# Performance work log

Measured on AMD Instinct MI355X. Metric: run time of the kernel, lower is better.

The kernel has to match this reference:

```python
import jax, jax.numpy as jnp
import numpy as np


def setup_inputs() -> dict:
    key = jax.random.key(0)
    ks = jax.random.split(key, 4)
    B, T, D, H, E = 4, 2048, 1024, 4096, 8
    s = 0.02
    x = jax.random.normal(ks[0], (B, T, D), dtype=jnp.float32)
    Wr = jax.random.normal(ks[1], (D, E), dtype=jnp.float32) * s
    br = jnp.zeros((E,), dtype=jnp.float32)
    W1 = jax.random.normal(ks[2], (E, D, H), dtype=jnp.float32) * s
    b1 = jnp.zeros((E, H), dtype=jnp.float32)
    W2 = jax.random.normal(ks[3], (E, H, D), dtype=jnp.float32) * s
    b2 = jnp.zeros((E, D), dtype=jnp.float32)
    return {"x": x, "Wr": Wr, "br": br, "W1": W1, "b1": b1, "W2": W2, "b2": b2}


def reference(x, Wr, br, W1, b1, W2, b2):
    # Router: top-1 selection
    logits = jnp.einsum('btd,de->bte', x, Wr) + br            # [B,T,E]
    probs = jax.nn.softmax(logits, axis=-1)                   # [B,T,E]
    expert_idx = jnp.argmax(probs, axis=-1)                   # [B,T] int
    E = W1.shape[0]
    onehot = jax.nn.one_hot(expert_idx, E, dtype=x.dtype)     # [B,T,E]
    # Dense grouped-MLP over all experts, then combine with one-hot routing.
    # h: [B,E,T,H]
    h = jax.nn.relu(jnp.einsum('btd,edh->beth', x, W1) + b1[None, :, None, :])
    y = jnp.einsum('beth,ehd->betd', h, W2) + b2[None, :, None, :]  # [B,E,T,D]
    out = jnp.einsum('bte,betd->btd', onehot, y)              # [B,T,D]
    return out, probs, expert_idx
```

## Files before the change

### kernel.cpp

```cpp
#include <hip/hip_runtime.h>

#define NTOK 8192
#define DD 1024
#define HH 4096
#define EE 8
#define MAXBLK 72

typedef __attribute__((ext_vector_type(8))) short bf16x8;
typedef __attribute__((ext_vector_type(4))) float f32x4;

__device__ __forceinline__ unsigned short f2bf(float f) {
  unsigned u = __builtin_bit_cast(unsigned, f);
  u += 0x7fffu + ((u >> 16) & 1u);
  return (unsigned short)(u >> 16);
}

union Pack8 {
  unsigned short u[8];
  uint4 v;
};

__device__ __forceinline__ void gload_lds16(const void* g, void* l) {
  __builtin_amdgcn_global_load_lds(
      (const __attribute__((address_space(1))) unsigned int*)g,
      (__attribute__((address_space(3))) unsigned int*)l, 16, 0, 0);
}

__global__ __launch_bounds__(256) void k_router(
    const float* __restrict__ x, const float* __restrict__ Wr,
    const float* __restrict__ br, float* __restrict__ probs,
    float* __restrict__ idxf, int* __restrict__ idxi,
    unsigned short* __restrict__ xb) {
  const int lane = threadIdx.x & 63;
  const int token = blockIdx.x * 4 + (threadIdx.x >> 6);
  const float* xr = x + (size_t)token * DD;

  float acc[EE];
#pragma unroll
  for (int e = 0; e < EE; ++e) acc[e] = 0.f;

#pragma unroll
  for (int i = 0; i < 4; ++i) {
    const int d0 = i * 256 + lane * 4;
    const float4 xv = *reinterpret_cast<const float4*>(xr + d0);
    union { unsigned short u[4]; uint2 v; } pk;
    pk.u[0] = f2bf(xv.x); pk.u[1] = f2bf(xv.y);
    pk.u[2] = f2bf(xv.z); pk.u[3] = f2bf(xv.w);
    *reinterpret_cast<uint2*>(xb + (size_t)token * DD + d0) = pk.v;
    const float xs[4] = {xv.x, xv.y, xv.z, xv.w};
#pragma unroll
    for (int j = 0; j < 4; ++j) {
      const float xd = xs[j];
      const float4 w0 = *reinterpret_cast<const float4*>(Wr + (size_t)(d0 + j) * EE);
      const float4 w1 = *reinterpret_cast<const float4*>(Wr + (size_t)(d0 + j) * EE + 4);
      acc[0] += xd * w0.x; acc[1] += xd * w0.y; acc[2] += xd * w0.z; acc[3] += xd * w0.w;
      acc[4] += xd * w1.x; acc[5] += xd * w1.y; acc[6] += xd * w1.z; acc[7] += xd * w1.w;
    }
  }
#pragma unroll
  for (int s = 32; s > 0; s >>= 1) {
#pragma unroll
    for (int e = 0; e < EE; ++e) acc[e] += __shfl_xor(acc[e], s, 64);
  }

  float lg[EE];
#pragma unroll
  for (int e = 0; e < EE; ++e) lg[e] = acc[e] + br[e];

  int best = 0;
  float bv = lg[0];
#pragma unroll
  for (int e = 1; e < EE; ++e) {
    if (lg[e] > bv) { bv = lg[e]; best = e; }
  }
  float p[EE], s = 0.f;
#pragma unroll
  for (int e = 0; e < EE; ++e) { p[e] = expf(lg[e] - bv); s += p[e]; }
  const float inv = 1.f / s;

  if (lane == 0) {
#pragma unroll
    for (int e = 0; e < EE; ++e) probs[(size_t)token * EE + e] = p[e] * inv;
    idxf[token] = (float)best;
    idxi[token] = best;
  }
}

__global__ __launch_bounds__(512) void k_compact(const int* __restrict__ idxi,
                                                 int* __restrict__ cnt,
                                                 int* __restrict__ off,
                                                 int* __restrict__ sorted,
                                                 int* __restrict__ meta) {
  __shared__ int sidx[NTOK];
  __shared__ int scnt[EE], soff[EE];
  const int tid = threadIdx.x;
  for (int i = tid; i < NTOK; i += 512) sidx[i] = idxi[i];
  __syncthreads();
  const int w = tid >> 6, lane = tid & 63;
  if (w < EE) {
    int c = 0;
    for (int i = 0; i < NTOK / 64; ++i) {
      unsigned long long m = __ballot(sidx[i * 64 + lane] == w);
      c += __popcll(m);
    }
    if (lane == 0) scnt[w] = c;
  }
  __syncthreads();
  if (tid == 0) {
    int s = 0;
    for (int e = 0; e < EE; ++e) { soff[e] = s; s += scnt[e]; }
    int nb = 0;
    for (int e = 0; e < EE; ++e) {
      const int nmb = (scnt[e] + 127) >> 7;
      for (int m = 0; m < nmb; ++m) {
        meta[16 + nb] = e;
        meta[96 + nb] = m << 7;
        ++nb;
      }
    }
    meta[0] = nb;
  }
  __syncthreads();
  if (w < EE) {
    int base = soff[w];
    const unsigned long long ltmask = (1ull << lane) - 1ull;
    for (int i = 0; i < NTOK / 64; ++i) {
      const int tok = i * 64 + lane;
      const bool f = (sidx[tok] == w);
      unsigned long long m = __ballot(f);
      if (f) {
        int r = __popcll(m & ltmask);
        sorted[base + r] = tok;
      }
      base += __popcll(m);
    }
    if (lane == 0) { cnt[w] = scnt[w]; off[w] = soff[w]; }
  }
}

__global__ __launch_bounds__(256) void k_trcvt64(const float* __restrict__ in,
                                                 unsigned short* __restrict__ outp,
                                                 int R, int C) {
  const int e = blockIdx.z;
  const int r0 = blockIdx.y * 64, c0 = blockIdx.x * 64;
  const float* src = in + (size_t)e * R * C + (size_t)r0 * C + c0;
  unsigned short* dst = outp + (size_t)e * R * C + (size_t)c0 * R + r0;
  __shared__ unsigned short t[64 * 66];
  const int tid = threadIdx.x;
#pragma unroll
  for (int it = 0; it < 4; ++it) {
    const int r = it * 16 + (tid >> 4), c4 = (tid & 15) * 4;
    const float4 v = *reinterpret_cast<const float4*>(src + (size_t)r * C + c4);
    t[r * 66 + c4 + 0] = f2bf(v.x);
    t[r * 66 + c4 + 1] = f2bf(v.y);
    t[r * 66 + c4 + 2] = f2bf(v.z);
    t[r * 66 + c4 + 3] = f2bf(v.w);
  }
  __syncthreads();
#pragma unroll
  for (int it = 0; it < 2; ++it) {
    const int cc = it * 32 + (tid >> 3), r8 = (tid & 7) * 8;
    Pack8 p;
#pragma unroll
    for (int j = 0; j < 8; ++j) p.u[j] = t[(r8 + j) * 66 + cc];
    *reinterpret_cast<uint4*>(dst + (size_t)cc * R + r8) = p.v;
  }
}

__global__ __launch_bounds__(256) void k_gemm1n(
    const unsigned short* __restrict__ xb, const unsigned short* __restrict__ W1t,
    const float* __restrict__ b1, const int* __restrict__ meta,
    const int* __restrict__ cnt, const int* __restrict__ off,
    const int* __restrict__ sorted, unsigned short* __restrict__ h) {
  const int bid = blockIdx.y;
  if (bid >= meta[0]) return;
  const int e = meta[16 + bid];
  const int m0 = meta[96 + bid];
  const int c = cnt[e], base = off[e];
  const int n0 = blockIdx.x * 128;

  __shared__ __align__(16) unsigned short Al[128 * 64];
  __shared__ __align__(16) unsigned short Bl[128 * 64];

  const int tid = threadIdx.x, l = tid & 63, w = tid >> 6;

  const unsigned short* aptr[4];
  const unsigned short* bptr[4];
  int soff4[4];
#pragma unroll
  for (int i = 0; i < 4; ++i) {
    const int r = i * 32 + w * 8 + (l >> 3);
    const int swz = ((l & 7) ^ (r & 7)) * 8;
    int ar = m0 + r; if (ar >= c) ar = c - 1;
    const int tok = sorted[base + ar];
    aptr[i] = xb + (size_t)tok * DD + swz;
    bptr[i] = W1t + ((size_t)e * HH + n0 + r) * DD + swz;
    soff4[i] = r * 64 + (l & 7) * 8;
  }

  const int lr = l & 15, lg = l >> 4;
  const int wr = w >> 1, wc = w & 1;
  int aoff[4], boff[4], asw[4], bsw[4];
#pragma unroll
  for (int m = 0; m < 4; ++m) {
    int row = wr * 64 + m * 16 + lr;
    aoff[m] = row * 64; asw[m] = row & 7;
    row = wc * 64 + m * 16 + lr;
    boff[m] = row * 64; bsw[m] = row & 7;
  }

  f32x4 acc[4][4];
#pragma unroll
  for (int m = 0; m < 4; ++m)
#pragma unroll
    for (int n = 0; n < 4; ++n) acc[m][n] = {0.f, 0.f, 0.f, 0.f};

  for (int k0 = 0; k0 < DD; k0 += 64) {
    __syncthreads();
#pragma unroll
    for (int i = 0; i < 4; ++i) gload_lds16(aptr[i] + k0, &Al[soff4[i]]);
#pragma unroll
    for (int i = 0; i < 4; ++i) gload_lds16(bptr[i] + k0, &Bl[soff4[i]]);
    __syncthreads();
#pragma unroll
    for (int ks = 0; ks < 2; ++ks) {
      bf16x8 af[4], bv[4];
#pragma unroll
      for (int m = 0; m < 4; ++m)
        af[m] = *reinterpret_cast<const bf16x8*>(&Al[aoff[m] + (((ks * 4 + lg) ^ asw[m]) * 8)]);
#pragma unroll
      for (int n = 0; n < 4; ++n)
        bv[n] = *reinterpret_cast<const bf16x8*>(&Bl[boff[n] + (((ks * 4 + lg) ^ bsw[n]) * 8)]);
#pragma unroll
      for (int m = 0; m < 4; ++m)
#pragma unroll
        for (int n = 0; n < 4; ++n)
          acc[m][n] = __builtin_amdgcn_mfma_f32_16x16x32_bf16(af[m], bv[n], acc[m][n], 0, 0, 0);
    }
  }

  const int valid = c - m0;
#pragma unroll
  for (int m = 0; m < 4; ++m) {
#pragma unroll
    for (int rr = 0; rr < 4; ++rr) {
      const int tr = wr * 64 + m * 16 + lg * 4 + rr;
      if (tr < valid) {
        const size_t row = (size_t)(base + m0 + tr);
#pragma unroll
        for (int n = 0; n < 4; ++n) {
          const int col = n0 + wc * 64 + n * 16 + lr;
          const float v = acc[m][n][rr] + b1[e * HH + col];
          h[row * HH + col] = f2bf(fmaxf(v, 0.f));
        }
      }
    }
  }
}

template <int KH>
__global__ __launch_bounds__(256) void k_gemm2s(
    const unsigned short* __restrict__ h, const unsigned short* __restrict__ W2t,
    const float* __restrict__ b2, const int* __restrict__ meta,
    const int* __restrict__ cnt, const int* __restrict__ off,
    const int* __restrict__ sorted, float* __restrict__ out,
    float* __restrict__ scr) {
  const int bid = blockIdx.y;
  if (bid >= meta[0]) return;
  const int e = meta[16 + bid];
  const int m0 = meta[96 + bid];
  const int c = cnt[e], base = off[e];
  const int n0 = blockIdx.x * 64;
  const int kh = (KH == 2) ? blockIdx.z : 0;
  const int kbase = kh * (HH / KH);

  __shared__ __align__(16) unsigned short Al0[128 * 64];
  __shared__ __align__(16) unsigned short Al1[128 * 64];
  __shared__ __align__(16) unsigned short Bl0[64 * 64];
  __shared__ __align__(16) unsigned short Bl1[64 * 64];

  const int tid = threadIdx.x, l = tid & 63, w = tid >> 6;

  const unsigned short* aptr[4];
  const unsigned short* bptr[2];
  int asoff[4], bsoff[2];
#pragma unroll
  for (int i = 0; i < 4; ++i) {
    const int r = i * 32 + w * 8 + (l >> 3);
    const int swz = ((l & 7) ^ (r & 7)) * 8;
    int ar = m0 + r; if (ar >= c) ar = c - 1;
    aptr[i] = h + (size_t)(base + ar) * HH + kbase + swz;
    asoff[i] = r * 64 + (l & 7) * 8;
  }
#pragma unroll
  for (int i = 0; i < 2; ++i) {
    const int r = i * 32 + w * 8 + (l >> 3);
    const int swz = ((l & 7) ^ (r & 7)) * 8;
    bptr[i] = W2t + ((size_t)e * DD + n0 + r) * HH + kbase + swz;
    bsoff[i] = r * 64 + (l & 7) * 8;
  }

  const int lr = l & 15, lg = l >> 4;
  const int wr = w >> 1, wc = w & 1;
  int aoff[4], boff[2], asw[4], bsw[2];
#pragma unroll
  for (int m = 0; m < 4; ++m) {
    const int row = wr * 64 + m * 16 + lr;
    aoff[m] = row * 64; asw[m] = row & 7;
  }
#pragma unroll
  for (int n = 0; n < 2; ++n) {
    const int row = wc * 32 + n * 16 + lr;
    boff[n] = row * 64; bsw[n] = row & 7;
  }

  f32x4 acc[4][2];
#pragma unroll
  for (int m = 0; m < 4; ++m)
#pragma unroll
    for (int n = 0; n < 2; ++n) acc[m][n] = {0.f, 0.f, 0.f, 0.f};

  for (int k0 = 0; k0 < HH / KH; k0 += 128) {
    __syncthreads();
#pragma unroll
    for (int i = 0; i < 4; ++i) gload_lds16(aptr[i] + k0, &Al0[asoff[i]]);
#pragma unroll
    for (int i = 0; i < 4; ++i) gload_lds16(aptr[i] + k0 + 64, &Al1[asoff[i]]);
#pragma unroll
    for (int i = 0; i < 2; ++i) gload_lds16(bptr[i] + k0, &Bl0[bsoff[i]]);
#pragma unroll
    for (int i = 0; i < 2; ++i) gload_lds16(bptr[i] + k0 + 64, &Bl1[bsoff[i]]);
    __syncthreads();
#pragma unroll
    for (int ks = 0; ks < 2; ++ks) {
      bf16x8 af[4], bv[2];
#pragma unroll
      for (int m = 0; m < 4; ++m)
        af[m] = *reinterpret_cast<const bf16x8*>(&Al0[aoff[m] + (((ks * 4 + lg) ^ asw[m]) * 8)]);
#pragma unroll
      for (int n = 0; n < 2; ++n)
        bv[n] = *reinterpret_cast<const bf16x8*>(&Bl0[boff[n] + (((ks * 4 + lg) ^ bsw[n]) * 8)]);
#pragma unroll
      for (int m = 0; m < 4; ++m)
#pragma unroll
        for (int n = 0; n < 2; ++n)
          acc[m][n] = __builtin_amdgcn_mfma_f32_16x16x32_bf16(af[m], bv[n], acc[m][n], 0, 0, 0);
    }
#pragma unroll
    for (int ks = 0; ks < 2; ++ks) {
      bf16x8 af[4], bv[2];
#pragma unroll
      for (int m = 0; m < 4; ++m)
        af[m] = *reinterpret_cast<const bf16x8*>(&Al1[aoff[m] + (((ks * 4 + lg) ^ asw[m]) * 8)]);
#pragma unroll
      for (int n = 0; n < 2; ++n)
        bv[n] = *reinterpret_cast<const bf16x8*>(&Bl1[boff[n] + (((ks * 4 + lg) ^ bsw[n]) * 8)]);
#pragma unroll
      for (int m = 0; m < 4; ++m)
#pragma unroll
        for (int n = 0; n < 2; ++n)
          acc[m][n] = __builtin_amdgcn_mfma_f32_16x16x32_bf16(af[m], bv[n], acc[m][n], 0, 0, 0);
    }
  }

  float* dst = (KH == 2 && blockIdx.z == 1) ? scr : out;
  const int valid = c - m0;
#pragma unroll
  for (int m = 0; m < 4; ++m) {
#pragma unroll
    for (int rr = 0; rr < 4; ++rr) {
      const int tr = wr * 64 + m * 16 + lg * 4 + rr;
      if (tr < valid) {
        const int token = sorted[base + m0 + tr];
#pragma unroll
        for (int n = 0; n < 2; ++n) {
          const int col = n0 + wc * 32 + n * 16 + lr;
          float v = acc[m][n][rr];
          if (KH == 1) v += b2[e * DD + col];
          dst[(size_t)token * DD + col] = v;
        }
      }
    }
  }
}

__global__ __launch_bounds__(256) void k_reduce2(float* __restrict__ out,
                                                 const float* __restrict__ scr,
                                                 const float* __restrict__ b2,
                                                 const int* __restrict__ idxi) {
  const size_t f = (size_t)blockIdx.x * 256 + threadIdx.x;
  const int token = (int)(f >> 8);
  const int d4 = ((int)f & 255) * 4;
  const int e = idxi[token];
  const float4 a = *reinterpret_cast<const float4*>(out + f * 4);
  const float4 b = *reinterpret_cast<const float4*>(scr + f * 4);
  const float4 bb = *reinterpret_cast<const float4*>(b2 + (size_t)e * DD + d4);
  float4 r;
  r.x = a.x + b.x + bb.x;
  r.y = a.y + b.y + bb.y;
  r.z = a.z + b.z + bb.z;
  r.w = a.w + b.w + bb.w;
  *reinterpret_cast<float4*>(out + f * 4) = r;
}

extern "C" void kernel_launch(void* const* d_in, const int* in_sizes, int n_in,
                              void* d_out, int out_size, void* d_ws, size_t ws_size,
                              hipStream_t stream) {
  const float* x  = (const float*)d_in[0];
  const float* Wr = (const float*)d_in[1];
  const float* br = (const float*)d_in[2];
  const float* W1 = (const float*)d_in[3];
  const float* b1 = (const float*)d_in[4];
  const float* W2 = (const float*)d_in[5];
  const float* b2 = (const float*)d_in[6];

  float* out   = (float*)d_out;
  float* probs = out + (size_t)NTOK * DD;
  float* idxf  = probs + (size_t)NTOK * EE;

  char* ws = (char*)d_ws;
  int* cnt    = (int*)(ws + 0);
  int* off    = (int*)(ws + 64);
  int* meta   = (int*)(ws + 128);
  int* idxi   = (int*)(ws + 1024);
  int* sorted = (int*)(ws + 33792);

  const size_t OFF_XB  = 66560;
  const size_t OFF_W1T = OFF_XB + (size_t)NTOK * DD * 2;
  const size_t OFF_H   = OFF_W1T + (size_t)EE * DD * HH * 2;
  const size_t OFF_W2T = OFF_XB;
  const size_t OFF_SCR = OFF_H + (size_t)NTOK * HH * 2;
  const size_t NEED_SPLIT = OFF_SCR + (size_t)NTOK * DD * 4;

  unsigned short* xb  = (unsigned short*)(ws + OFF_XB);
  unsigned short* W1t = (unsigned short*)(ws + OFF_W1T);
  unsigned short* W2t = (unsigned short*)(ws + OFF_W2T);
  unsigned short* h   = (unsigned short*)(ws + OFF_H);
  float*          scr = (float*)(ws + OFF_SCR);

  k_router<<<NTOK / 4, 256, 0, stream>>>(x, Wr, br, probs, idxf, idxi, xb);
  k_compact<<<1, 512, 0, stream>>>(idxi, cnt, off, sorted, meta);
  k_trcvt64<<<dim3(HH / 64, DD / 64, EE), 256, 0, stream>>>(W1, W1t, DD, HH);
  k_gemm1n<<<dim3(HH / 128, MAXBLK), 256, 0, stream>>>(xb, W1t, b1, meta, cnt, off, sorted, h);
  k_trcvt64<<<dim3(DD / 64, HH / 64, EE), 256, 0, stream>>>(W2, W2t, HH, DD);

  if (ws_size >= NEED_SPLIT) {
    k_gemm2s<2><<<dim3(DD / 64, MAXBLK, 2), 256, 0, stream>>>(
        h, W2t, b2, meta, cnt, off, sorted, out, scr);
    k_reduce2<<<(NTOK * DD) / (256 * 4), 256, 0, stream>>>(out, scr, b2, idxi);
  } else {
    k_gemm2s<1><<<dim3(DD / 64, MAXBLK, 1), 256, 0, stream>>>(
        h, W2t, b2, meta, cnt, off, sorted, out, scr);
  }
}
```

Measured before the change: 377.7 us.

## Fuse weight transposes into router and first GEMM launches for overlap

The W1 transpose-and-convert blocks are appended to the router kernel's grid, and the W2 transpose blocks are appended to the first expert GEMM's grid. Independent work then runs alongside compute-bound work instead of in separate serialized launches. W2t moves to its own workspace region so it no longer aliases xb, which needs a larger workspace; smaller workspaces fall back to separate launches. Merging the grids also makes the GEMM kernel's shared memory a union sized for both block roles.

```diff
diff --git a/kernel.cpp b/kernel.cpp
--- a/kernel.cpp
+++ b/kernel.cpp
@@ -26,63 +26,102 @@
       (__attribute__((address_space(3))) unsigned int*)l, 16, 0, 0);
 }
 
-__global__ __launch_bounds__(256) void k_router(
+__device__ __forceinline__ void trcvt_body(const float* __restrict__ src0,
+                                           unsigned short* __restrict__ dst0,
+                                           int R, int C, int r0, int c0,
+                                           unsigned short* t) {
+  const int tid = threadIdx.x;
+  const float* src = src0 + (size_t)r0 * C + c0;
+  unsigned short* dst = dst0 + (size_t)c0 * R + r0;
+#pragma unroll
+  for (int it = 0; it < 4; ++it) {
+    const int r = it * 16 + (tid >> 4), c4 = (tid & 15) * 4;
+    const float4 v = *reinterpret_cast<const float4*>(src + (size_t)r * C + c4);
+    t[r * 66 + c4 + 0] = f2bf(v.x);
+    t[r * 66 + c4 + 1] = f2bf(v.y);
+    t[r * 66 + c4 + 2] = f2bf(v.z);
+    t[r * 66 + c4 + 3] = f2bf(v.w);
+  }
+  __syncthreads();
+#pragma unroll
+  for (int it = 0; it < 2; ++it) {
+    const int cc = it * 32 + (tid >> 3), r8 = (tid & 7) * 8;
+    Pack8 p;
+#pragma unroll
+    for (int j = 0; j < 8; ++j) p.u[j] = t[(r8 + j) * 66 + cc];
+    *reinterpret_cast<uint4*>(dst + (size_t)cc * R + r8) = p.v;
+  }
+}
+
+__global__ __launch_bounds__(256) void k_rtr1(
     const float* __restrict__ x, const float* __restrict__ Wr,
     const float* __restrict__ br, float* __restrict__ probs,
     float* __restrict__ idxf, int* __restrict__ idxi,
-    unsigned short* __restrict__ xb) {
-  const int lane = threadIdx.x & 63;
-  const int token = blockIdx.x * 4 + (threadIdx.x >> 6);
-  const float* xr = x + (size_t)token * DD;
-
-  float acc[EE];
-#pragma unroll
-  for (int e = 0; e < EE; ++e) acc[e] = 0.f;
-
-#pragma unroll
-  for (int i = 0; i < 4; ++i) {
-    const int d0 = i * 256 + lane * 4;
-    const float4 xv = *reinterpret_cast<const float4*>(xr + d0);
-    union { unsigned short u[4]; uint2 v; } pk;
-    pk.u[0] = f2bf(xv.x); pk.u[1] = f2bf(xv.y);
-    pk.u[2] = f2bf(xv.z); pk.u[3] = f2bf(xv.w);
-    *reinterpret_cast<uint2*>(xb + (size_t)token * DD + d0) = pk.v;
-    const float xs[4] = {xv.x, xv.y, xv.z, xv.w};
-#pragma unroll
-    for (int j = 0; j < 4; ++j) {
-      const float xd = xs[j];
-      const float4 w0 = *reinterpret_cast<const float4*>(Wr + (size_t)(d0 + j) * EE);
-      const float4 w1 = *reinterpret_cast<const float4*>(Wr + (size_t)(d0 + j) * EE + 4);
-      acc[0] += xd * w0.x; acc[1] += xd * w0.y; acc[2] += xd * w0.z; acc[3] += xd * w0.w;
-      acc[4] += xd * w1.x; acc[5] += xd * w1.y; acc[6] += xd * w1.z; acc[7] += xd * w1.w;
-    }
-  }
-#pragma unroll
-  for (int s = 32; s > 0; s >>= 1) {
-#pragma unroll
-    for (int e = 0; e < EE; ++e) acc[e] += __shfl_xor(acc[e], s, 64);
-  }
-
-  float lg[EE];
-#pragma unroll
-  for (int e = 0; e < EE; ++e) lg[e] = acc[e] + br[e];
-
-  int best = 0;
-  float bv = lg[0];
-#pragma unroll
-  for (int e = 1; e < EE; ++e) {
-    if (lg[e] > bv) { bv = lg[e]; best = e; }
-  }
-  float p[EE], s = 0.f;
-#pragma unroll
-  for (int e = 0; e < EE; ++e) { p[e] = expf(lg[e] - bv); s += p[e]; }
-  const float inv = 1.f / s;
-
-  if (lane == 0) {
-#pragma unroll
-    for (int e = 0; e < EE; ++e) probs[(size_t)token * EE + e] = p[e] * inv;
-    idxf[token] = (float)best;
-    idxi[token] = best;
+    unsigned short* __restrict__ xb,
+    const float* __restrict__ W1, unsigned short* __restrict__ W1t) {
+  __shared__ __align__(16) unsigned short SH[64 * 66];
+  const int bid = blockIdx.x;
+  if (bid < NTOK / 4) {
+    const int lane = threadIdx.x & 63;
+    const int token = bid * 4 + (threadIdx.x >> 6);
+    const float* xr = x + (size_t)token * DD;
+
+    float acc[EE];
+#pragma unroll
+    for (int e = 0; e < EE; ++e) acc[e] = 0.f;
+
+#pragma unroll
+    for (int i = 0; i < 4; ++i) {
+      const int d0 = i * 256 + lane * 4;
+      const float4 xv = *reinterpret_cast<const float4*>(xr + d0);
+      union { unsigned short u[4]; uint2 v; } pk;
+      pk.u[0] = f2bf(xv.x); pk.u[1] = f2bf(xv.y);
+      pk.u[2] = f2bf(xv.z); pk.u[3] = f2bf(xv.w);
+      *reinterpret_cast<uint2*>(xb + (size_t)token * DD + d0) = pk.v;
+      const float xs[4] = {xv.x, xv.y, xv.z, xv.w};
+#pragma unroll
+      for (int j = 0; j < 4; ++j) {
+        const float xd = xs[j];
+        const float4 w0 = *reinterpret_cast<const float4*>(Wr + (size_t)(d0 + j) * EE);
+        const float4 w1 = *reinterpret_cast<const float4*>(Wr + (size_t)(d0 + j) * EE + 4);
+        acc[0] += xd * w0.x; acc[1] += xd * w0.y; acc[2] += xd * w0.z; acc[3] += xd * w0.w;
+        acc[4] += xd * w1.x; acc[5] += xd * w1.y; acc[6] += xd * w1.z; acc[7] += xd * w1.w;
+      }
+    }
+#pragma unroll
+    for (int s = 32; s > 0; s >>= 1) {
+#pragma unroll
+      for (int e = 0; e < EE; ++e) acc[e] += __shfl_xor(acc[e], s, 64);
+    }
+
+    float lg[EE];
+#pragma unroll
+    for (int e = 0; e < EE; ++e) lg[e] = acc[e] + br[e];
+
+    int best = 0;
+    float bv = lg[0];
+#pragma unroll
+    for (int e = 1; e < EE; ++e) {
+      if (lg[e] > bv) { bv = lg[e]; best = e; }
+    }
+    float p[EE], s = 0.f;
+#pragma unroll
+    for (int e = 0; e < EE; ++e) { p[e] = expf(lg[e] - bv); s += p[e]; }
+    const float inv = 1.f / s;
+
+    if (lane == 0) {
+#pragma unroll
+      for (int e = 0; e < EE; ++e) probs[(size_t)token * EE + e] = p[e] * inv;
+      idxf[token] = (float)best;
+      idxi[token] = best;
+    }
+  } else {
+    const int t = bid - NTOK / 4;
+    const int e = t >> 10;
+    const int rem = t & 1023;
+    const int c0 = (rem & 63) * 64;
+    const int r0 = (rem >> 6) * 64;
+    trcvt_body(W1 + (size_t)e * DD * HH, W1t + (size_t)e * DD * HH, DD, HH, r0, c0, SH);
   }
 }
 
@@ -141,37 +180,28 @@
 __global__ __launch_bounds__(256) void k_trcvt64(const float* __restrict__ in,
                                                  unsigned short* __restrict__ outp,
                                                  int R, int C) {
+  __shared__ unsigned short t[64 * 66];
   const int e = blockIdx.z;
-  const int r0 = blockIdx.y * 64, c0 = blockIdx.x * 64;
-  const float* src = in + (size_t)e * R * C + (size_t)r0 * C + c0;
-  unsigned short* dst = outp + (size_t)e * R * C + (size_t)c0 * R + r0;
-  __shared__ unsigned short t[64 * 66];
-  const int tid = threadIdx.x;
-#pragma unroll
-  for (int it = 0; it < 4; ++it) {
-    const int r = it * 16 + (tid >> 4), c4 = (tid & 15) * 4;
-    const float4 v = *reinterpret_cast<const float4*>(src + (size_t)r * C + c4);
-    t[r * 66 + c4 + 0] = f2bf(v.x);
-    t[r * 66 + c4 + 1] = f2bf(v.y);
-    t[r * 66 + c4 + 2] = f2bf(v.z);
-    t[r * 66 + c4 + 3] = f2bf(v.w);
-  }
-  __syncthreads();
-#pragma unroll
-  for (int it = 0; it < 2; ++it) {
-    const int cc = it * 32 + (tid >> 3), r8 = (tid & 7) * 8;
-    Pack8 p;
-#pragma unroll
-    for (int j = 0; j < 8; ++j) p.u[j] = t[(r8 + j) * 66 + cc];
-    *reinterpret_cast<uint4*>(dst + (size_t)cc * R + r8) = p.v;
-  }
-}
-
-__global__ __launch_bounds__(256) void k_gemm1n(
+  trcvt_body(in + (size_t)e * R * C, outp + (size_t)e * R * C, R, C,
+             blockIdx.y * 64, blockIdx.x * 64, t);
+}
+
+__global__ __launch_bounds__(256) void k_g1tr2(
     const unsigned short* __restrict__ xb, const unsigned short* __restrict__ W1t,
     const float* __restrict__ b1, const int* __restrict__ meta,
     const int* __restrict__ cnt, const int* __restrict__ off,
-    const int* __restrict__ sorted, unsigned short* __restrict__ h) {
+    const int* __restrict__ sorted, unsigned short* __restrict__ h,
+    const float* __restrict__ W2, unsigned short* __restrict__ W2t) {
+  __shared__ __align__(16) unsigned short SH[2 * 128 * 64];
+  if (blockIdx.y >= MAXBLK) {
+    const int t = (blockIdx.y - MAXBLK) * 32 + blockIdx.x;
+    const int e = t >> 10;
+    const int rem = t & 1023;
+    const int c0 = (rem & 15) * 64;
+    const int r0 = (rem >> 4) * 64;
+    trcvt_body(W2 + (size_t)e * HH * DD, W2t + (size_t)e * HH * DD, HH, DD, r0, c0, SH);
+    return;
+  }
   const int bid = blockIdx.y;
   if (bid >= meta[0]) return;
   const int e = meta[16 + bid];
@@ -179,8 +209,8 @@
   const int c = cnt[e], base = off[e];
   const int n0 = blockIdx.x * 128;
 
-  __shared__ __align__(16) unsigned short Al[128 * 64];
-  __shared__ __align__(16) unsigned short Bl[128 * 64];
+  unsigned short* Al = SH;
+  unsigned short* Bl = SH + 128 * 64;
 
   const int tid = threadIdx.x, l = tid & 63, w = tid >> 6;
 
@@ -425,30 +455,42 @@
   int* idxi   = (int*)(ws + 1024);
   int* sorted = (int*)(ws + 33792);
 
-  const size_t OFF_XB  = 66560;
-  const size_t OFF_W1T = OFF_XB + (size_t)NTOK * DD * 2;
-  const size_t OFF_H   = OFF_W1T + (size_t)EE * DD * HH * 2;
-  const size_t OFF_W2T = OFF_XB;
-  const size_t OFF_SCR = OFF_H + (size_t)NTOK * HH * 2;
-  const size_t NEED_SPLIT = OFF_SCR + (size_t)NTOK * DD * 4;
+  const size_t OFF_XB   = 66560;
+  const size_t OFF_W1T  = OFF_XB + (size_t)NTOK * DD * 2;
+  const size_t OFF_H    = OFF_W1T + (size_t)EE * DD * HH * 2;
+  const size_t OFF_SCR  = OFF_H + (size_t)NTOK * HH * 2;
+  const size_t OFF_W2TB = OFF_SCR + (size_t)NTOK * DD * 4;
+  const size_t NEED_SPLIT = OFF_W2TB;
+  const size_t NEED_BIG   = OFF_W2TB + (size_t)EE * DD * HH * 2;
 
   unsigned short* xb  = (unsigned short*)(ws + OFF_XB);
   unsigned short* W1t = (unsigned short*)(ws + OFF_W1T);
-  unsigned short* W2t = (unsigned short*)(ws + OFF_W2T);
   unsigned short* h   = (unsigned short*)(ws + OFF_H);
   float*          scr = (float*)(ws + OFF_SCR);
 
-  k_router<<<NTOK / 4, 256, 0, stream>>>(x, Wr, br, probs, idxf, idxi, xb);
+  k_rtr1<<<NTOK / 4 + 8192, 256, 0, stream>>>(x, Wr, br, probs, idxf, idxi, xb, W1, W1t);
   k_compact<<<1, 512, 0, stream>>>(idxi, cnt, off, sorted, meta);
-  k_trcvt64<<<dim3(HH / 64, DD / 64, EE), 256, 0, stream>>>(W1, W1t, DD, HH);
-  k_gemm1n<<<dim3(HH / 128, MAXBLK), 256, 0, stream>>>(xb, W1t, b1, meta, cnt, off, sorted, h);
-  k_trcvt64<<<dim3(DD / 64, HH / 64, EE), 256, 0, stream>>>(W2, W2t, HH, DD);
-
-  if (ws_size >= NEED_SPLIT) {
+
+  if (ws_size >= NEED_BIG) {
+    unsigned short* W2t = (unsigned short*)(ws + OFF_W2TB);
+    k_g1tr2<<<dim3(HH / 128, MAXBLK + 256), 256, 0, stream>>>(
+        xb, W1t, b1, meta, cnt, off, sorted, h, W2, W2t);
+    k_gemm2s<2><<<dim3(DD / 64, MAXBLK, 2), 256, 0, stream>>>(
+        h, W2t, b2, meta, cnt, off, sorted, out, scr);
+    k_reduce2<<<(NTOK * DD) / (256 * 4), 256, 0, stream>>>(out, scr, b2, idxi);
+  } else if (ws_size >= NEED_SPLIT) {
+    unsigned short* W2t = (unsigned short*)(ws + OFF_XB);
+    k_g1tr2<<<dim3(HH / 128, MAXBLK), 256, 0, stream>>>(
+        xb, W1t, b1, meta, cnt, off, sorted, h, W2, W2t);
+    k_trcvt64<<<dim3(DD / 64, HH / 64, EE), 256, 0, stream>>>(W2, W2t, HH, DD);
     k_gemm2s<2><<<dim3(DD / 64, MAXBLK, 2), 256, 0, stream>>>(
         h, W2t, b2, meta, cnt, off, sorted, out, scr);
     k_reduce2<<<(NTOK * DD) / (256 * 4), 256, 0, stream>>>(out, scr, b2, idxi);
   } else {
+    unsigned short* W2t = (unsigned short*)(ws + OFF_XB);
+    k_g1tr2<<<dim3(HH / 128, MAXBLK), 256, 0, stream>>>(
+        xb, W1t, b1, meta, cnt, off, sorted, h, W2, W2t);
+    k_trcvt64<<<dim3(DD / 64, HH / 64, EE), 256, 0, stream>>>(W2, W2t, HH, DD);
     k_gemm2s<1><<<dim3(DD / 64, MAXBLK, 1), 256, 0, stream>>>(
         h, W2t, b2, meta, cnt, off, sorted, out, scr);
   }
```

New measurement: 373.8 us, median of 2. About the same (-1.0%).
